# Kernel optimization log

Measured on AMD Instinct MI355X. Metric: run time of the kernel, lower is better.

The kernel has to match this reference:

```python
import jax, jax.numpy as jnp
import numpy as np

N = 50000      # nodes
E = 800000     # edges (avg degree 16)
F_IN = 128     # num_node_features
H = 128        # hidden_channels


def setup_inputs() -> dict:
    key = jax.random.key(0)
    ks = jax.random.split(key, 9)
    x = jax.random.normal(ks[0], (N, F_IN), jnp.float32)
    edge_index = jax.random.randint(ks[1], (2, E), 0, N, dtype=jnp.int64)
    s_in = 1.0 / np.sqrt(F_IN)
    s_h = 1.0 / np.sqrt(H)
    return {
        "x": x,
        "edge_index": edge_index,
        "W1": jax.random.normal(ks[2], (F_IN, H), jnp.float32) * s_in,
        "b1": jax.random.normal(ks[3], (H,), jnp.float32) * 0.01,
        "W2": jax.random.normal(ks[4], (H, H), jnp.float32) * s_h,
        "b2": jax.random.normal(ks[5], (H,), jnp.float32) * 0.01,
        "W3": jax.random.normal(ks[6], (H, H), jnp.float32) * s_h,
        "b3": jax.random.normal(ks[7], (H,), jnp.float32) * 0.01,
    }


def gcn_layer(x, src_f, dst_f, dinv, W, b):
    # PyG GCNConv: out = D^-1/2 (A+I) D^-1/2 (x @ W) + b
    h = x @ W                                   # [N, H]
    coef = dinv[src_f] * dinv[dst_f]            # [E+N]
    msg = coef[:, None] * h[src_f]              # gather + scale, [E+N, H]
    agg = jax.ops.segment_sum(msg, dst_f, num_segments=x.shape[0])
    return agg + b


def reference(x, edge_index, W1, b1, W2, b2, W3, b3):
    n = x.shape[0]
    loops = jnp.arange(n, dtype=edge_index.dtype)
    src_f = jnp.concatenate([edge_index[0], loops])  # edges + self loops
    dst_f = jnp.concatenate([edge_index[1], loops])
    # degree with unit edge weights (edge_weight=None)
    deg = jax.ops.segment_sum(jnp.ones(src_f.shape[0], x.dtype), dst_f, num_segments=n)
    dinv = jnp.where(deg > 0, jax.lax.rsqrt(deg), 0.0)
    h = jax.nn.relu(gcn_layer(x, src_f, dst_f, dinv, W1, b1))
    # dropout p=0.1 is identity in eval mode
    h = jax.nn.relu(gcn_layer(h, src_f, dst_f, dinv, W2, b2))
    return gcn_layer(h, src_f, dst_f, dinv, W3, b3)
```

## Files before the change

### kernel.cpp

```cpp
#include <hip/hip_runtime.h>

#define HDIM 128
#define BM 64
#define CAP 64

typedef _Float16 half8 __attribute__((ext_vector_type(8)));
typedef _Float16 half2v __attribute__((ext_vector_type(2)));
typedef float f32x4 __attribute__((ext_vector_type(4)));


__global__ void fill_k(const int* __restrict__ src, const int* __restrict__ dst,
                       int* __restrict__ cur, int* __restrict__ slots, int E) {
    int e = blockIdx.x * blockDim.x + threadIdx.x;
    if (e >= E) return;
    int s = src[e], d = dst[e];
    int p = atomicAdd(&cur[d], 1);
    if (p < CAP) slots[(size_t)d * CAP + p] = s;
}

__global__ void dinv_k(const int* __restrict__ cnt, float* __restrict__ dinv, int n) {
    int i = blockIdx.x * blockDim.x + threadIdx.x;
    if (i < n) dinv[i] = rsqrtf((float)(cnt[i] + 1));
}

__global__ void cvt_w_k(const float* __restrict__ W, _Float16* __restrict__ Wp) {
    int i = blockIdx.x * 256 + threadIdx.x;
    int k = i >> 7, col = i & 127;
    Wp[((size_t)(k >> 3) * 128 + col) * 8 + (k & 7)] = (_Float16)W[i];
}


template <bool A32>
__global__ __launch_bounds__(256) void gemm_h(const void* __restrict__ Ain,
                                              const _Float16* __restrict__ Wp,
                                              _Float16* __restrict__ C, int n) {
    const int lane = threadIdx.x & 63;
    const int wave = threadIdx.x >> 6;
    const int row0 = blockIdx.x * BM + wave * 16;
    const int rlo  = lane & 15;
    const int khi  = lane >> 4;

    f32x4 acc[8] = {};

#pragma unroll
    for (int s = 0; s < 4; ++s) {
        half8 a = {};
        int arow = row0 + rlo;
        if (arow < n) {
            if constexpr (A32) {
                const float* Af = (const float*)Ain;
                const float4* p0 = (const float4*)&Af[(size_t)arow * HDIM + 32 * s + 8 * khi];
                float4 lo = p0[0], hi = p0[1];
                a[0] = (_Float16)lo.x; a[1] = (_Float16)lo.y;
                a[2] = (_Float16)lo.z; a[3] = (_Float16)lo.w;
                a[4] = (_Float16)hi.x; a[5] = (_Float16)hi.y;
                a[6] = (_Float16)hi.z; a[7] = (_Float16)hi.w;
            } else {
                a = *(const half8*)&((const _Float16*)Ain)[(size_t)arow * HDIM + 32 * s + 8 * khi];
            }
        }
        const int kb = 4 * s + khi;
#pragma unroll
        for (int c = 0; c < 8; ++c) {
            half8 b = *(const half8*)&Wp[((size_t)kb * HDIM + 16 * c + rlo) * 8];
            acc[c] = __builtin_amdgcn_mfma_f32_16x16x32_f16(a, b, acc[c], 0, 0, 0);
        }
    }

#pragma unroll
    for (int c = 0; c < 8; ++c) {
        int col = 16 * c + rlo;
#pragma unroll
        for (int r = 0; r < 4; ++r) {
            int row = row0 + khi * 4 + r;
            if (row < n) C[(size_t)row * HDIM + col] = (_Float16)acc[c][r];
        }
    }
}


__global__ __launch_bounds__(256) void agg_h(const _Float16* __restrict__ h,
                                             const int* __restrict__ cnt,
                                             const int* __restrict__ slots,
                                             const float* __restrict__ dinv,
                                             const float* __restrict__ bias,
                                             _Float16* __restrict__ out16,
                                             float* __restrict__ out32,
                                             int n, int relu) {
    int node = blockIdx.x * 4 + (threadIdx.x >> 6);
    int lane = threadIdx.x & 63;
    if (node >= n) return;

    const half2v* hp = (const half2v*)h;
    float di = dinv[node];
    half2v sv = hp[(size_t)node * 64 + lane];
    float ax = di * (float)sv[0];
    float ay = di * (float)sv[1];

    const int* el = &slots[(size_t)node * CAP];
    int deg = cnt[node];
    if (deg > CAP) deg = CAP;

    int e = 0;
    for (; e + 8 <= deg; e += 8) {
        int s[8];
#pragma unroll
        for (int u = 0; u < 8; ++u) s[u] = el[e + u];
        float ds[8];
        half2v v[8];
#pragma unroll
        for (int u = 0; u < 8; ++u) {
            ds[u] = dinv[s[u]];
            v[u]  = hp[(size_t)s[u] * 64 + lane];
        }
#pragma unroll
        for (int u = 0; u < 8; ++u) {
            ax += ds[u] * (float)v[u][0];
            ay += ds[u] * (float)v[u][1];
        }
    }
    for (; e < deg; ++e) {
        int sc = el[e];
        float ds = dinv[sc];
        half2v v = hp[(size_t)sc * 64 + lane];
        ax += ds * (float)v[0];
        ay += ds * (float)v[1];
    }

    float2 b = ((const float2*)bias)[lane];
    ax = di * ax + b.x;
    ay = di * ay + b.y;
    if (relu) { ax = fmaxf(ax, 0.f); ay = fmaxf(ay, 0.f); }

    if (out16) {
        half2v o = { (_Float16)ax, (_Float16)ay };
        ((half2v*)out16)[(size_t)node * 64 + lane] = o;
    } else {
        float2 o; o.x = ax; o.y = ay;
        ((float2*)out32)[(size_t)node * 64 + lane] = o;
    }
}


extern "C" void kernel_launch(void* const* d_in, const int* in_sizes, int n_in,
                              void* d_out, int out_size, void* d_ws, size_t ws_size,
                              hipStream_t stream) {
    const float* x  = (const float*)d_in[0];
    const int*   ei = (const int*)d_in[1];
    const float* W1 = (const float*)d_in[2];
    const float* b1 = (const float*)d_in[3];
    const float* W2 = (const float*)d_in[4];
    const float* b2 = (const float*)d_in[5];
    const float* W3 = (const float*)d_in[6];
    const float* b3 = (const float*)d_in[7];
    float* out = (float*)d_out;

    const int n = in_sizes[0] / HDIM;
    const int E = in_sizes[1] / 2;
    const int* src = ei;
    const int* dst = ei + E;

    char* p = (char*)d_ws;
    auto alloc = [&](size_t bytes) {
        char* r = p;
        p += (bytes + 255) & ~(size_t)255;
        return r;
    };
    float*     dinv  = (float*)alloc((size_t)n * 4);
    int*       cnt   = (int*)  alloc((size_t)n * 4);
    int*       slots = (int*)  alloc((size_t)n * CAP * 4);
    _Float16*  Wp1   = (_Float16*)alloc(HDIM * HDIM * 2);
    _Float16*  Wp2   = (_Float16*)alloc(HDIM * HDIM * 2);
    _Float16*  Wp3   = (_Float16*)alloc(HDIM * HDIM * 2);
    _Float16*  bufA  = (_Float16*)alloc(((size_t)n + 64) * HDIM * 2);
    _Float16*  bufG  = (_Float16*)alloc(((size_t)n + 64) * HDIM * 2);

    hipMemsetAsync(cnt, 0, (size_t)n * 4, stream);
    fill_k<<<(E + 255) / 256, 256, 0, stream>>>(src, dst, cnt, slots, E);
    dinv_k<<<(n + 255) / 256, 256, 0, stream>>>(cnt, dinv, n);

    cvt_w_k<<<64, 256, 0, stream>>>(W1, Wp1);
    cvt_w_k<<<64, 256, 0, stream>>>(W2, Wp2);
    cvt_w_k<<<64, 256, 0, stream>>>(W3, Wp3);

    const int gb = (n + BM - 1) / BM;
    const int ab = (n + 3) / 4;

    gemm_h<true><<<gb, 256, 0, stream>>>(x, Wp1, bufG, n);
    agg_h<<<ab, 256, 0, stream>>>(bufG, cnt, slots, dinv, b1, bufA, nullptr, n, 1);
    gemm_h<false><<<gb, 256, 0, stream>>>(bufA, Wp2, bufG, n);
    agg_h<<<ab, 256, 0, stream>>>(bufG, cnt, slots, dinv, b2, bufA, nullptr, n, 1);
    gemm_h<false><<<gb, 256, 0, stream>>>(bufA, Wp3, bufG, n);
    agg_h<<<ab, 256, 0, stream>>>(bufG, cnt, slots, dinv, b3, nullptr, out, n, 0);
}
```

Measured before the change: 304.5 us.

## Fold source-side dinv into GEMM epilogue, pad degree counters, fuse prep kernels

The GEMM epilogue now scales each row by its own rsqrt(deg+1), so the aggregation kernel no longer has to gather dinv for every neighbor and just sums pre-scaled features. The degree counters are spread out to one per 64 bytes so atomics on different nodes do not share a cache line. The memset, the dinv kernel and the three weight-conversion kernels are merged into one prep kernel, cutting launches. In exchange the counter array is 16x larger to zero, and each node's degree is recomputed with rsqrt in both the GEMM and the aggregation.

Measured after the change: 291.5 us. 1.04x faster.

```diff
diff --git a/kernel.cpp b/kernel.cpp
--- a/kernel.cpp
+++ b/kernel.cpp
@@ -3,36 +3,45 @@
 #define HDIM 128
 #define BM 64
 #define CAP 64
+#define CSH 4
 
 typedef _Float16 half8 __attribute__((ext_vector_type(8)));
 typedef _Float16 half2v __attribute__((ext_vector_type(2)));
 typedef float f32x4 __attribute__((ext_vector_type(4)));
 
 
+__global__ void prep_k(const float* __restrict__ W1, const float* __restrict__ W2,
+                       const float* __restrict__ W3,
+                       _Float16* __restrict__ Wp1, _Float16* __restrict__ Wp2,
+                       _Float16* __restrict__ Wp3,
+                       int* __restrict__ cntp, int n) {
+    int i = blockIdx.x * blockDim.x + threadIdx.x;
+    int stride = gridDim.x * blockDim.x;
+    for (int j = i; j < (n << CSH); j += stride) cntp[j] = 0;
+    for (int j = i; j < HDIM * HDIM; j += stride) {
+        int k = j >> 7, col = j & 127;
+        size_t p = ((size_t)(k >> 3) * HDIM + col) * 8 + (k & 7);
+        Wp1[p] = (_Float16)W1[j];
+        Wp2[p] = (_Float16)W2[j];
+        Wp3[p] = (_Float16)W3[j];
+    }
+}
+
+
 __global__ void fill_k(const int* __restrict__ src, const int* __restrict__ dst,
-                       int* __restrict__ cur, int* __restrict__ slots, int E) {
+                       int* __restrict__ cntp, int* __restrict__ slots, int E) {
     int e = blockIdx.x * blockDim.x + threadIdx.x;
     if (e >= E) return;
     int s = src[e], d = dst[e];
-    int p = atomicAdd(&cur[d], 1);
+    int p = atomicAdd(&cntp[d << CSH], 1);
     if (p < CAP) slots[(size_t)d * CAP + p] = s;
-}
-
-__global__ void dinv_k(const int* __restrict__ cnt, float* __restrict__ dinv, int n) {
-    int i = blockIdx.x * blockDim.x + threadIdx.x;
-    if (i < n) dinv[i] = rsqrtf((float)(cnt[i] + 1));
-}
-
-__global__ void cvt_w_k(const float* __restrict__ W, _Float16* __restrict__ Wp) {
-    int i = blockIdx.x * 256 + threadIdx.x;
-    int k = i >> 7, col = i & 127;
-    Wp[((size_t)(k >> 3) * 128 + col) * 8 + (k & 7)] = (_Float16)W[i];
 }
 
 
 template <bool A32>
 __global__ __launch_bounds__(256) void gemm_h(const void* __restrict__ Ain,
                                               const _Float16* __restrict__ Wp,
+                                              const int* __restrict__ cntp,
                                               _Float16* __restrict__ C, int n) {
     const int lane = threadIdx.x & 63;
     const int wave = threadIdx.x >> 6;
@@ -67,22 +76,28 @@
         }
     }
 
+    float dr[4];
+#pragma unroll
+    for (int r = 0; r < 4; ++r) {
+        int row = row0 + khi * 4 + r;
+        dr[r] = (row < n) ? rsqrtf((float)(cntp[row << CSH] + 1)) : 0.f;
+    }
+
 #pragma unroll
     for (int c = 0; c < 8; ++c) {
         int col = 16 * c + rlo;
 #pragma unroll
         for (int r = 0; r < 4; ++r) {
             int row = row0 + khi * 4 + r;
-            if (row < n) C[(size_t)row * HDIM + col] = (_Float16)acc[c][r];
+            if (row < n) C[(size_t)row * HDIM + col] = (_Float16)(dr[r] * acc[c][r]);
         }
     }
 }
 
 
 __global__ __launch_bounds__(256) void agg_h(const _Float16* __restrict__ h,
-                                             const int* __restrict__ cnt,
+                                             const int* __restrict__ cntp,
                                              const int* __restrict__ slots,
-                                             const float* __restrict__ dinv,
                                              const float* __restrict__ bias,
                                              _Float16* __restrict__ out16,
                                              float* __restrict__ out32,
@@ -92,39 +107,34 @@
     if (node >= n) return;
 
     const half2v* hp = (const half2v*)h;
-    float di = dinv[node];
+    int deg = cntp[node << CSH];
+    float di = rsqrtf((float)(deg + 1));
+    if (deg > CAP) deg = CAP;
+
     half2v sv = hp[(size_t)node * 64 + lane];
-    float ax = di * (float)sv[0];
-    float ay = di * (float)sv[1];
+    float ax = (float)sv[0];
+    float ay = (float)sv[1];
 
     const int* el = &slots[(size_t)node * CAP];
-    int deg = cnt[node];
-    if (deg > CAP) deg = CAP;
 
     int e = 0;
     for (; e + 8 <= deg; e += 8) {
         int s[8];
 #pragma unroll
         for (int u = 0; u < 8; ++u) s[u] = el[e + u];
-        float ds[8];
         half2v v[8];
 #pragma unroll
-        for (int u = 0; u < 8; ++u) {
-            ds[u] = dinv[s[u]];
-            v[u]  = hp[(size_t)s[u] * 64 + lane];
-        }
+        for (int u = 0; u < 8; ++u) v[u] = hp[(size_t)s[u] * 64 + lane];
 #pragma unroll
         for (int u = 0; u < 8; ++u) {
-            ax += ds[u] * (float)v[u][0];
-            ay += ds[u] * (float)v[u][1];
+            ax += (float)v[u][0];
+            ay += (float)v[u][1];
         }
     }
     for (; e < deg; ++e) {
-        int sc = el[e];
-        float ds = dinv[sc];
-        half2v v = hp[(size_t)sc * 64 + lane];
-        ax += ds * (float)v[0];
-        ay += ds * (float)v[1];
+        half2v v = hp[(size_t)el[e] * 64 + lane];
+        ax += (float)v[0];
+        ay += (float)v[1];
     }
 
     float2 b = ((const float2*)bias)[lane];
@@ -166,8 +176,7 @@
         p += (bytes + 255) & ~(size_t)255;
         return r;
     };
-    float*     dinv  = (float*)alloc((size_t)n * 4);
-    int*       cnt   = (int*)  alloc((size_t)n * 4);
+    int*       cntp  = (int*)  alloc(((size_t)n << CSH) * 4);
     int*       slots = (int*)  alloc((size_t)n * CAP * 4);
     _Float16*  Wp1   = (_Float16*)alloc(HDIM * HDIM * 2);
     _Float16*  Wp2   = (_Float16*)alloc(HDIM * HDIM * 2);
@@ -175,21 +184,16 @@
     _Float16*  bufA  = (_Float16*)alloc(((size_t)n + 64) * HDIM * 2);
     _Float16*  bufG  = (_Float16*)alloc(((size_t)n + 64) * HDIM * 2);
 
-    hipMemsetAsync(cnt, 0, (size_t)n * 4, stream);
-    fill_k<<<(E + 255) / 256, 256, 0, stream>>>(src, dst, cnt, slots, E);
-    dinv_k<<<(n + 255) / 256, 256, 0, stream>>>(cnt, dinv, n);
-
-    cvt_w_k<<<64, 256, 0, stream>>>(W1, Wp1);
-    cvt_w_k<<<64, 256, 0, stream>>>(W2, Wp2);
-    cvt_w_k<<<64, 256, 0, stream>>>(W3, Wp3);
+    prep_k<<<1024, 256, 0, stream>>>(W1, W2, W3, Wp1, Wp2, Wp3, cntp, n);
+    fill_k<<<(E + 255) / 256, 256, 0, stream>>>(src, dst, cntp, slots, E);
 
     const int gb = (n + BM - 1) / BM;
     const int ab = (n + 3) / 4;
 
-    gemm_h<true><<<gb, 256, 0, stream>>>(x, Wp1, bufG, n);
-    agg_h<<<ab, 256, 0, stream>>>(bufG, cnt, slots, dinv, b1, bufA, nullptr, n, 1);
-    gemm_h<false><<<gb, 256, 0, stream>>>(bufA, Wp2, bufG, n);
-    agg_h<<<ab, 256, 0, stream>>>(bufG, cnt, slots, dinv, b2, bufA, nullptr, n, 1);
-    gemm_h<false><<<gb, 256, 0, stream>>>(bufA, Wp3, bufG, n);
-    agg_h<<<ab, 256, 0, stream>>>(bufG, cnt, slots, dinv, b3, nullptr, out, n, 0);
+    gemm_h<true><<<gb, 256, 0, stream>>>(x, Wp1, cntp, bufG, n);
+    agg_h<<<ab, 256, 0, stream>>>(bufG, cntp, slots, b1, bufA, nullptr, n, 1);
+    gemm_h<false><<<gb, 256, 0, stream>>>(bufA, Wp2, cntp, bufG, n);
+    agg_h<<<ab, 256, 0, stream>>>(bufG, cntp, slots, b2, bufA, nullptr, n, 1);
+    gemm_h<false><<<gb, 256, 0, stream>>>(bufA, Wp3, cntp, bufG, n);
+    agg_h<<<ab, 256, 0, stream>>>(bufG, cntp, slots, b3, nullptr, out, n, 0);
 }
```
